# Optimization experiments

Hardware: AMD Instinct MI355X
Metric: run time of the kernel (lower is better)

## Reference

```python
import jax, jax.numpy as jnp
import numpy as np

N = 20000      # nodes
E = 320000     # edges (avg degree 16)
HID = 128      # hidden_channel
OUT = 128      # output_channel
SEQ = 8


def setup_inputs() -> dict:
    key = jax.random.key(0)
    ks = jax.random.split(key, 8)
    h = jax.random.normal(ks[0], (N, HID), jnp.float32)
    c = jax.random.normal(ks[1], (N, HID), jnp.float32)
    edge_index = jax.random.randint(ks[2], (2, E), 0, N, jnp.int64)
    edge_attr = jax.random.uniform(ks[3], (E,), jnp.float32)
    # GCNConv weights (PyG: x @ W then propagate), xavier-ish scale
    W_init = jax.random.normal(ks[4], (2 * HID, 2 * OUT), jnp.float32) * (2.0 / (2 * HID + 2 * OUT)) ** 0.5
    b_init = jnp.zeros((2 * OUT,), jnp.float32)
    W_cell = jax.random.normal(ks[5], (HID + OUT, 4 * OUT), jnp.float32) * (2.0 / (HID + OUT + 4 * OUT)) ** 0.5
    b_cell = jnp.zeros((4 * OUT,), jnp.float32)
    return {"h": h, "c": c, "edge_index": edge_index, "edge_attr": edge_attr,
            "W_init": W_init, "b_init": b_init, "W_cell": W_cell, "b_cell": b_cell,
            "seq_len": SEQ}


def _gcn(x, W, b, src, dst, ew, dinv):
    # PyG GCNConv with normalize=True, add_self_loops=True (self-loop weight 1.0)
    xw = x @ W                                   # [N, C_out]
    norm = dinv[src] * ew * dinv[dst]            # sym-normalized edge weights
    agg = jnp.zeros_like(xw).at[dst].add(xw[src] * norm[:, None])
    agg = agg + xw * (dinv * dinv)[:, None]      # self-loop term
    return agg + b


def reference(h, c, edge_index, edge_attr, W_init, b_init, W_cell, b_cell, seq_len):
    src, dst = edge_index[0], edge_index[1]
    n = h.shape[0]
    # degree with self-loops (weight 1.0), shared by both convs
    deg = jnp.zeros((n,), h.dtype).at[dst].add(edge_attr) + 1.0
    dinv = jax.lax.rsqrt(deg)

    # _init_states
    states = jax.nn.elu(_gcn(jnp.concatenate([h, c], axis=1), W_init, b_init, src, dst, edge_attr, dinv))
    h_t, c_t = states[:, :OUT], states[:, OUT:]

    def step(carry, _):
        h_cur, c_cur = carry
        # NOTE: original code feeds the initial h (not h_cur) as x each step
        combined = jnp.concatenate([h, h_cur], axis=1)
        cc = _gcn(combined, W_cell, b_cell, src, dst, edge_attr, dinv)
        cc_i, cc_f, cc_o, cc_g = jnp.split(cc, 4, axis=1)
        c_next = jax.nn.sigmoid(cc_f) * c_cur + jax.nn.sigmoid(cc_i) * jnp.tanh(cc_g)
        h_next = jax.nn.sigmoid(cc_o) * jnp.tanh(c_next)
        return (h_next, c_next), h_next

    (_, _), out = jax.lax.scan(step, (h_t, c_t), None, length=seq_len)
    return out  # [seq_len, N, OUT]
```

## Files before the change

kernel.cpp:

```cpp
#include <hip/hip_runtime.h>

#define N_NODES 20000
#define N_EDGES 320000
#define SEQ 8

typedef __attribute__((ext_vector_type(8))) short bf16x8;
typedef __attribute__((ext_vector_type(4))) float floatx4;
typedef const unsigned int __attribute__((address_space(1)))* gas_u32;
typedef unsigned int __attribute__((address_space(3)))* las_u32;

__device__ __forceinline__ unsigned short f2bf(float f) {
  unsigned int u = __builtin_bit_cast(unsigned int, f);
  return (unsigned short)((u + 0x7fffu + ((u >> 16) & 1u)) >> 16);
}
__device__ __forceinline__ float bflo(unsigned int u) {
  return __builtin_bit_cast(float, u << 16);
}
__device__ __forceinline__ float bfhi(unsigned int u) {
  return __builtin_bit_cast(float, u & 0xffff0000u);
}
__device__ __forceinline__ float sigf(float x) { return 1.f / (1.f + __expf(-x)); }

__device__ __forceinline__ void gl_lds16(const void* g, void* l) {
  auto gp = (gas_u32)g;
  auto lp = (las_u32)(unsigned int)(unsigned long long)l;
  __builtin_amdgcn_global_load_lds(gp, lp, 16, 0, 0);
}


__global__ void k_prologue(const float* __restrict__ Wi,
                           const float* __restrict__ Wc,
                           const float* __restrict__ bc,
                           unsigned short* __restrict__ WiT,
                           unsigned short* __restrict__ WcT,
                           float* __restrict__ bcp,
                           float* __restrict__ deg, int* __restrict__ counts) {
  int idx = blockIdx.x * 256 + threadIdx.x;
  if (idx < N_NODES) { deg[idx] = 1.0f; counts[idx] = 0; }
  if (idx < 65536) {
    int n = idx >> 8, k = idx & 255;
    WiT[n * 256 + k] = f2bf(Wi[k * 256 + n]);
  }
  if (idx < 512) bcp[idx] = bc[((idx & 3) << 7) | (idx >> 2)];
  int n2 = idx >> 8, k2 = idx & 255;
  int orig = ((n2 & 3) << 7) | (n2 >> 2);
  WcT[n2 * 256 + k2] = f2bf(Wc[k2 * 512 + orig]);
}

__global__ void k_deg(const int* __restrict__ ei, const float* __restrict__ ea,
                      float* __restrict__ deg, int* __restrict__ counts) {
  int e = blockIdx.x * 256 + threadIdx.x;
  if (e >= N_EDGES) return;
  int d = ei[N_EDGES + e];
  atomicAdd(&deg[d], ea[e]);
  atomicAdd(&counts[d], 1);
}

__global__ __launch_bounds__(1024) void k_scan(
    const int* __restrict__ counts, const float* __restrict__ deg,
    float* __restrict__ dinv, int* __restrict__ row_ptr,
    int* __restrict__ cursor) {
  __shared__ int smw[16];
  int t = threadIdx.x;
  int lane = t & 63, wv = t >> 6;
  int base = t * 20;
  int v[20];
  float dv[20];
  bool live = (t < 1000);
  if (live) {
    const int4* pc = (const int4*)(counts + base);
    const float4* pd = (const float4*)(deg + base);
#pragma unroll
    for (int i = 0; i < 5; ++i) {
      int4 q = pc[i];
      float4 f = pd[i];
      v[4 * i] = q.x; v[4 * i + 1] = q.y; v[4 * i + 2] = q.z; v[4 * i + 3] = q.w;
      dv[4 * i] = f.x; dv[4 * i + 1] = f.y; dv[4 * i + 2] = f.z; dv[4 * i + 3] = f.w;
    }
  } else {
#pragma unroll
    for (int i = 0; i < 20; ++i) { v[i] = 0; dv[i] = 1.f; }
  }
  int s = 0;
#pragma unroll
  for (int i = 0; i < 20; ++i) s += v[i];
  int inc = s;
#pragma unroll
  for (int o = 1; o < 64; o <<= 1) {
    int u = __shfl_up(inc, o);
    if (lane >= o) inc += u;
  }
  if (lane == 63) smw[wv] = inc;
  __syncthreads();
  if (t == 0) {
    int r = 0;
#pragma unroll
    for (int i = 0; i < 16; ++i) { int x = smw[i]; smw[i] = r; r += x; }
  }
  __syncthreads();
  int run = smw[wv] + inc - s;
  if (live) {
    int rp[20];
    float iv[20];
#pragma unroll
    for (int i = 0; i < 20; ++i) {
      rp[i] = run;
      run += v[i];
      iv[i] = rsqrtf(dv[i]);
    }
    int4* prp = (int4*)(row_ptr + base);
    int4* pcu = (int4*)(cursor + base);
    float4* pdv = (float4*)(dinv + base);
#pragma unroll
    for (int i = 0; i < 5; ++i) {
      int4 q; q.x = rp[4 * i]; q.y = rp[4 * i + 1]; q.z = rp[4 * i + 2]; q.w = rp[4 * i + 3];
      prp[i] = q;
      pcu[i] = q;
      float4 f; f.x = iv[4 * i]; f.y = iv[4 * i + 1]; f.z = iv[4 * i + 2]; f.w = iv[4 * i + 3];
      pdv[i] = f;
    }
  }
  if (t == 0) row_ptr[N_NODES] = N_EDGES;
}

__global__ void k_fill(const int* __restrict__ ei, const float* __restrict__ ea,
                       const float* __restrict__ dinv, int* __restrict__ cursor,
                       int2* __restrict__ csr) {
  int e = blockIdx.x * 256 + threadIdx.x;
  if (e >= N_EDGES) return;
  int s = ei[e], d = ei[N_EDGES + e];
  int k = atomicAdd(&cursor[d], 1);
  int2 p;
  p.x = s;
  p.y = __builtin_bit_cast(int, dinv[s] * ea[e] * dinv[d]);
  csr[k] = p;
}


__global__ __launch_bounds__(256) void k_agg_init(
    const float* __restrict__ h, const float* __restrict__ c,
    unsigned int* __restrict__ AhAc_u, const float* __restrict__ dinv,
    const int* __restrict__ row_ptr, const int2* __restrict__ csr) {
  int wid = (blockIdx.x * 256 + threadIdx.x) >> 6;
  int lane = threadIdx.x & 63;
  if (wid >= N_NODES) return;
  float di = dinv[wid], dd = di * di;
  const float4* xb = (lane < 32) ? (const float4*)h : (const float4*)c;
  int lcol = lane & 31;
  float4 a = xb[(size_t)wid * 32 + lcol];
  float s0 = a.x * dd, s1 = a.y * dd, s2 = a.z * dd, s3 = a.w * dd;
  int e0 = row_ptr[wid], end = row_ptr[wid + 1];
  for (int base = e0; base < end; base += 64) {
    int n = end - base;
    if (n > 64) n = 64;
    int sl = 0;
    float wl = 0.f;
    if (base + lane < end) {
      int2 p = csr[base + lane];
      sl = p.x;
      wl = __builtin_bit_cast(float, p.y);
    }
    int j = 0;
    for (; j + 4 <= n; j += 4) {
      int sa = __shfl(sl, j), sb = __shfl(sl, j + 1);
      int sc = __shfl(sl, j + 2), sd = __shfl(sl, j + 3);
      float wa = __shfl(wl, j), wb = __shfl(wl, j + 1);
      float wc = __shfl(wl, j + 2), wd = __shfl(wl, j + 3);
      float4 va = xb[(size_t)sa * 32 + lcol];
      float4 vb = xb[(size_t)sb * 32 + lcol];
      float4 vc = xb[(size_t)sc * 32 + lcol];
      float4 vd = xb[(size_t)sd * 32 + lcol];
      s0 += va.x * wa; s1 += va.y * wa; s2 += va.z * wa; s3 += va.w * wa;
      s0 += vb.x * wb; s1 += vb.y * wb; s2 += vb.z * wb; s3 += vb.w * wb;
      s0 += vc.x * wc; s1 += vc.y * wc; s2 += vc.z * wc; s3 += vc.w * wc;
      s0 += vd.x * wd; s1 += vd.y * wd; s2 += vd.z * wd; s3 += vd.w * wd;
    }
    for (; j < n; ++j) {
      int sa = __shfl(sl, j);
      float wa = __shfl(wl, j);
      float4 va = xb[(size_t)sa * 32 + lcol];
      s0 += va.x * wa; s1 += va.y * wa; s2 += va.z * wa; s3 += va.w * wa;
    }
  }
  uint2 o;
  o.x = (unsigned int)f2bf(s0) | ((unsigned int)f2bf(s1) << 16);
  o.y = (unsigned int)f2bf(s2) | ((unsigned int)f2bf(s3) << 16);
  ((uint2*)AhAc_u)[(size_t)wid * 64 + lane] = o;
}

__global__ __launch_bounds__(256) void k_agg_step(
    const unsigned int* __restrict__ hbf_u, unsigned int* __restrict__ AhAc_u,
    const float* __restrict__ dinv, const int* __restrict__ row_ptr,
    const int2* __restrict__ csr) {
  int wid = (blockIdx.x * 256 + threadIdx.x) >> 6;
  int lane = threadIdx.x & 63;
  if (wid >= N_NODES) return;
  float di = dinv[wid], dd = di * di;
  unsigned int a = hbf_u[(size_t)wid * 64 + lane];
  float s0 = bflo(a) * dd, s1 = bfhi(a) * dd;
  int e0 = row_ptr[wid], end = row_ptr[wid + 1];
  for (int base = e0; base < end; base += 64) {
    int n = end - base;
    if (n > 64) n = 64;
    int sl = 0;
    float wl = 0.f;
    if (base + lane < end) {
      int2 p = csr[base + lane];
      sl = p.x;
      wl = __builtin_bit_cast(float, p.y);
    }
    int j = 0;
    for (; j + 4 <= n; j += 4) {
      int sa = __shfl(sl, j), sb = __shfl(sl, j + 1);
      int sc = __shfl(sl, j + 2), sd = __shfl(sl, j + 3);
      float wa = __shfl(wl, j), wb = __shfl(wl, j + 1);
      float wc = __shfl(wl, j + 2), wd = __shfl(wl, j + 3);
      unsigned int va = hbf_u[(size_t)sa * 64 + lane];
      unsigned int vb = hbf_u[(size_t)sb * 64 + lane];
      unsigned int vc = hbf_u[(size_t)sc * 64 + lane];
      unsigned int vd = hbf_u[(size_t)sd * 64 + lane];
      s0 += bflo(va) * wa; s1 += bfhi(va) * wa;
      s0 += bflo(vb) * wb; s1 += bfhi(vb) * wb;
      s0 += bflo(vc) * wc; s1 += bfhi(vc) * wc;
      s0 += bflo(vd) * wd; s1 += bfhi(vd) * wd;
    }
    for (; j < n; ++j) {
      int sa = __shfl(sl, j);
      float wa = __shfl(wl, j);
      unsigned int va = hbf_u[(size_t)sa * 64 + lane];
      s0 += bflo(va) * wa; s1 += bfhi(va) * wa;
    }
  }
  AhAc_u[(size_t)wid * 128 + 64 + lane] =
      (unsigned int)f2bf(s0) | ((unsigned int)f2bf(s1) << 16);
}

template <int EPI, int KK, int LDA>
__global__ __launch_bounds__(256) void k_gemm(
    const unsigned short* __restrict__ A, const unsigned short* __restrict__ BT,
    const float* __restrict__ bias,
    float* __restrict__ c_cur, unsigned short* __restrict__ hbf,
    float* __restrict__ out0) {
  __shared__ __align__(16) union {
    struct { unsigned short a[128 * 64]; unsigned short b[128 * 64]; } ab;
    float ep[64 * 132];
  } sm;
  const int M = N_NODES;
  int tid = threadIdx.x;
  int bm0 = blockIdx.x * 128, bn0 = blockIdx.y * 128;
  int wave = tid >> 6, lane = tid & 63;
  int wrow = (wave >> 1) * 64, wcol = (wave & 1) * 64;
  int lr = lane & 15, lq = lane >> 4;
  int key = lr & 7;

  int lr8 = lane >> 3, cq = lane & 7;
  int gq8 = (cq ^ lr8) * 8;

  floatx4 acc[4][4];
#pragma unroll
  for (int i = 0; i < 4; i++)
#pragma unroll
    for (int j = 0; j < 4; j++) acc[i][j] = (floatx4){0.f, 0.f, 0.f, 0.f};

  for (int k0 = 0; k0 < KK; k0 += 64) {
    __syncthreads();
#pragma unroll
    for (int p = 0; p < 4; ++p) {
      int row = p * 32 + wave * 8;
      int ra = bm0 + row + lr8;
      if (ra > M - 1) ra = M - 1;
      gl_lds16(A + (size_t)ra * LDA + k0 + gq8, sm.ab.a + row * 64);
      gl_lds16(BT + (size_t)(bn0 + row + lr8) * KK + k0 + gq8,
               sm.ab.b + row * 64);
    }
    __syncthreads();
#pragma unroll
    for (int ks = 0; ks < 2; ++ks) {
      int q = ks * 4 + lq;
      int slot = (q ^ key) << 3;
      bf16x8 af[4], bfr[4];
#pragma unroll
      for (int mi = 0; mi < 4; mi++)
        af[mi] = *(const bf16x8*)(sm.ab.a + (wrow + mi * 16 + lr) * 64 + slot);
#pragma unroll
      for (int ni = 0; ni < 4; ni++)
        bfr[ni] = *(const bf16x8*)(sm.ab.b + (wcol + ni * 16 + lr) * 64 + slot);
#pragma unroll
      for (int mi = 0; mi < 4; mi++)
#pragma unroll
        for (int ni = 0; ni < 4; ni++)
          acc[mi][ni] = __builtin_amdgcn_mfma_f32_16x16x32_bf16(
              af[mi], bfr[ni], acc[mi][ni], 0, 0, 0);
    }
  }
  __syncthreads();

  if (EPI == 0) {
#pragma unroll
    for (int mi = 0; mi < 4; mi++) {
#pragma unroll
      for (int r = 0; r < 4; r++) {
        int grow = bm0 + wrow + mi * 16 + lq * 4 + r;
        if (grow >= M) continue;
#pragma unroll
        for (int ni = 0; ni < 4; ni++) {
          int gcol = bn0 + wcol + ni * 16 + lr;
          float v = acc[mi][ni][r] + bias[gcol];
          v = (v > 0.f) ? v : expm1f(v);
          if (gcol < 128) hbf[(size_t)grow * 128 + gcol] = f2bf(v);
          else c_cur[(size_t)grow * 128 + gcol - 128] = v;
        }
      }
    }
  } else {
#pragma unroll
    for (int hch = 0; hch < 2; ++hch) {
      if ((wrow >> 6) == hch) {
#pragma unroll
        for (int mi = 0; mi < 4; mi++)
#pragma unroll
          for (int r = 0; r < 4; r++) {
            int row_l = mi * 16 + lq * 4 + r;
#pragma unroll
            for (int ni = 0; ni < 4; ni++)
              sm.ep[row_l * 132 + wcol + ni * 16 + lr] = acc[mi][ni][r];
          }
      }
      __syncthreads();
#pragma unroll
      for (int it = 0; it < 8; ++it) {
        int p = tid + it * 256;
        int row_l = p >> 5, j = p & 31;
        int grow = bm0 + hch * 64 + row_l;
        if (grow < M) {
          int jg = (bn0 >> 2) + j;
          const float* eb = sm.ep + row_l * 132 + 4 * j;
          float4 kb = *(const float4*)&bias[bn0 + 4 * j];
          float gi = eb[0] + kb.x;
          float gf = eb[1] + kb.y;
          float go = eb[2] + kb.z;
          float gg = eb[3] + kb.w;
          size_t o = (size_t)grow * 128 + jg;
          float cp = c_cur[o];
          float cn = sigf(gf) * cp + sigf(gi) * tanhf(gg);
          float hn = sigf(go) * tanhf(cn);
          c_cur[o] = cn;
          hbf[o] = f2bf(hn);
          out0[o] = hn;
        }
      }
      __syncthreads();
    }
  }
}

extern "C" void kernel_launch(void* const* d_in, const int* in_sizes, int n_in,
                              void* d_out, int out_size, void* d_ws, size_t ws_size,
                              hipStream_t stream) {
  const float* h  = (const float*)d_in[0];
  const float* c  = (const float*)d_in[1];
  const int*   ei = (const int*)d_in[2];
  const float* ea = (const float*)d_in[3];
  const float* Wi = (const float*)d_in[4];
  const float* bi = (const float*)d_in[5];
  const float* Wc = (const float*)d_in[6];
  const float* bc = (const float*)d_in[7];
  float* out = (float*)d_out;

  char* w = (char*)d_ws;
  size_t off = 0;
  auto alloc = [&](size_t bytes) {
    void* p = w + off;
    off += (bytes + 511) & ~(size_t)511;
    return p;
  };
  float* deg           = (float*)alloc(N_NODES * 4);
  float* dinv          = (float*)alloc(N_NODES * 4);
  int* counts          = (int*)alloc(N_NODES * 4);
  int* cursor          = (int*)alloc(N_NODES * 4);
  int* row_ptr         = (int*)alloc((N_NODES + 1) * 4);
  int2* csr            = (int2*)alloc((size_t)N_EDGES * 8);
  unsigned short* WiT  = (unsigned short*)alloc(256 * 256 * 2);
  unsigned short* WcT  = (unsigned short*)alloc(512 * 256 * 2);
  float* bcp           = (float*)alloc(512 * 4);
  unsigned short* AhAc = (unsigned short*)alloc((size_t)N_NODES * 256 * 2);
  unsigned short* hbf  = (unsigned short*)alloc((size_t)N_NODES * 128 * 2);
  float* c_cur         = (float*)alloc((size_t)N_NODES * 128 * 4);

  const int NB_E = (N_EDGES + 255) / 256;
  const int NB_AGG = N_NODES * 64 / 256;
  const int MB = (N_NODES + 127) / 128;

  k_prologue<<<512, 256, 0, stream>>>(Wi, Wc, bc, WiT, WcT, bcp, deg, counts);
  k_deg<<<NB_E, 256, 0, stream>>>(ei, ea, deg, counts);
  k_scan<<<1, 1024, 0, stream>>>(counts, deg, dinv, row_ptr, cursor);
  k_fill<<<NB_E, 256, 0, stream>>>(ei, ea, dinv, cursor, csr);

  k_agg_init<<<NB_AGG, 256, 0, stream>>>(h, c, (unsigned int*)AhAc, dinv,
                                         row_ptr, csr);
  k_gemm<0, 256, 256><<<dim3(MB, 2), 256, 0, stream>>>(
      AhAc, WiT, bi, c_cur, hbf, nullptr);

  for (int t = 0; t < SEQ; ++t) {
    k_agg_step<<<NB_AGG, 256, 0, stream>>>((unsigned int*)hbf,
                                           (unsigned int*)AhAc, dinv, row_ptr,
                                           csr);
    k_gemm<2, 256, 256><<<dim3(MB, 4), 256, 0, stream>>>(
        AhAc, WcT, bcp, c_cur, hbf, out + (size_t)t * N_NODES * 128);
  }
}
```

Measured before the change: 508.9 us.

## Fuse per-step aggregation, GEMM and LSTM epilogue into one kernel

Replaces the separate per-step aggregation kernel and gate GEMM with a single kernel. Each 128-row block first gathers neighbour h values into shared memory, then computes all four gate column tiles and applies the LSTM update. The hidden state is double-buffered because blocks now read the previous h while writing the new one. This removes the global round-trip of the aggregated h and one launch per step. In exchange, grid parallelism drops to about 157 blocks with large shared memory, and the latency-bound gather runs at low occupancy.

Result: slower. 819.5 us (+61.0%).

```diff
diff --git a/kernel.cpp b/kernel.cpp
--- a/kernel.cpp
+++ b/kernel.cpp
@@ -135,7 +135,6 @@
   p.y = __builtin_bit_cast(int, dinv[s] * ea[e] * dinv[d]);
   csr[k] = p;
 }
-
 
 __global__ __launch_bounds__(256) void k_agg_init(
     const float* __restrict__ h, const float* __restrict__ c,
@@ -188,63 +187,11 @@
   ((uint2*)AhAc_u)[(size_t)wid * 64 + lane] = o;
 }
 
-__global__ __launch_bounds__(256) void k_agg_step(
-    const unsigned int* __restrict__ hbf_u, unsigned int* __restrict__ AhAc_u,
-    const float* __restrict__ dinv, const int* __restrict__ row_ptr,
-    const int2* __restrict__ csr) {
-  int wid = (blockIdx.x * 256 + threadIdx.x) >> 6;
-  int lane = threadIdx.x & 63;
-  if (wid >= N_NODES) return;
-  float di = dinv[wid], dd = di * di;
-  unsigned int a = hbf_u[(size_t)wid * 64 + lane];
-  float s0 = bflo(a) * dd, s1 = bfhi(a) * dd;
-  int e0 = row_ptr[wid], end = row_ptr[wid + 1];
-  for (int base = e0; base < end; base += 64) {
-    int n = end - base;
-    if (n > 64) n = 64;
-    int sl = 0;
-    float wl = 0.f;
-    if (base + lane < end) {
-      int2 p = csr[base + lane];
-      sl = p.x;
-      wl = __builtin_bit_cast(float, p.y);
-    }
-    int j = 0;
-    for (; j + 4 <= n; j += 4) {
-      int sa = __shfl(sl, j), sb = __shfl(sl, j + 1);
-      int sc = __shfl(sl, j + 2), sd = __shfl(sl, j + 3);
-      float wa = __shfl(wl, j), wb = __shfl(wl, j + 1);
-      float wc = __shfl(wl, j + 2), wd = __shfl(wl, j + 3);
-      unsigned int va = hbf_u[(size_t)sa * 64 + lane];
-      unsigned int vb = hbf_u[(size_t)sb * 64 + lane];
-      unsigned int vc = hbf_u[(size_t)sc * 64 + lane];
-      unsigned int vd = hbf_u[(size_t)sd * 64 + lane];
-      s0 += bflo(va) * wa; s1 += bfhi(va) * wa;
-      s0 += bflo(vb) * wb; s1 += bfhi(vb) * wb;
-      s0 += bflo(vc) * wc; s1 += bfhi(vc) * wc;
-      s0 += bflo(vd) * wd; s1 += bfhi(vd) * wd;
-    }
-    for (; j < n; ++j) {
-      int sa = __shfl(sl, j);
-      float wa = __shfl(wl, j);
-      unsigned int va = hbf_u[(size_t)sa * 64 + lane];
-      s0 += bflo(va) * wa; s1 += bfhi(va) * wa;
-    }
-  }
-  AhAc_u[(size_t)wid * 128 + 64 + lane] =
-      (unsigned int)f2bf(s0) | ((unsigned int)f2bf(s1) << 16);
-}
-
-template <int EPI, int KK, int LDA>
-__global__ __launch_bounds__(256) void k_gemm(
+__global__ __launch_bounds__(256) void k_gemm0(
     const unsigned short* __restrict__ A, const unsigned short* __restrict__ BT,
-    const float* __restrict__ bias,
-    float* __restrict__ c_cur, unsigned short* __restrict__ hbf,
-    float* __restrict__ out0) {
-  __shared__ __align__(16) union {
-    struct { unsigned short a[128 * 64]; unsigned short b[128 * 64]; } ab;
-    float ep[64 * 132];
-  } sm;
+    const float* __restrict__ bias, float* __restrict__ c_cur,
+    unsigned short* __restrict__ hbf) {
+  __shared__ __align__(16) struct { unsigned short a[128 * 64]; unsigned short b[128 * 64]; } sm;
   const int M = N_NODES;
   int tid = threadIdx.x;
   int bm0 = blockIdx.x * 128, bn0 = blockIdx.y * 128;
@@ -252,7 +199,6 @@
   int wrow = (wave >> 1) * 64, wcol = (wave & 1) * 64;
   int lr = lane & 15, lq = lane >> 4;
   int key = lr & 7;
-
   int lr8 = lane >> 3, cq = lane & 7;
   int gq8 = (cq ^ lr8) * 8;
 
@@ -262,16 +208,15 @@
 #pragma unroll
     for (int j = 0; j < 4; j++) acc[i][j] = (floatx4){0.f, 0.f, 0.f, 0.f};
 
-  for (int k0 = 0; k0 < KK; k0 += 64) {
+  for (int k0 = 0; k0 < 256; k0 += 64) {
     __syncthreads();
 #pragma unroll
     for (int p = 0; p < 4; ++p) {
       int row = p * 32 + wave * 8;
       int ra = bm0 + row + lr8;
       if (ra > M - 1) ra = M - 1;
-      gl_lds16(A + (size_t)ra * LDA + k0 + gq8, sm.ab.a + row * 64);
-      gl_lds16(BT + (size_t)(bn0 + row + lr8) * KK + k0 + gq8,
-               sm.ab.b + row * 64);
+      gl_lds16(A + (size_t)ra * 256 + k0 + gq8, sm.a + row * 64);
+      gl_lds16(BT + (size_t)(bn0 + row + lr8) * 256 + k0 + gq8, sm.b + row * 64);
     }
     __syncthreads();
 #pragma unroll
@@ -281,10 +226,10 @@
       bf16x8 af[4], bfr[4];
 #pragma unroll
       for (int mi = 0; mi < 4; mi++)
-        af[mi] = *(const bf16x8*)(sm.ab.a + (wrow + mi * 16 + lr) * 64 + slot);
+        af[mi] = *(const bf16x8*)(sm.a + (wrow + mi * 16 + lr) * 64 + slot);
 #pragma unroll
       for (int ni = 0; ni < 4; ni++)
-        bfr[ni] = *(const bf16x8*)(sm.ab.b + (wcol + ni * 16 + lr) * 64 + slot);
+        bfr[ni] = *(const bf16x8*)(sm.b + (wcol + ni * 16 + lr) * 64 + slot);
 #pragma unroll
       for (int mi = 0; mi < 4; mi++)
 #pragma unroll
@@ -293,49 +238,176 @@
               af[mi], bfr[ni], acc[mi][ni], 0, 0, 0);
     }
   }
-  __syncthreads();
-
-  if (EPI == 0) {
-#pragma unroll
-    for (int mi = 0; mi < 4; mi++) {
-#pragma unroll
-      for (int r = 0; r < 4; r++) {
-        int grow = bm0 + wrow + mi * 16 + lq * 4 + r;
-        if (grow >= M) continue;
-#pragma unroll
-        for (int ni = 0; ni < 4; ni++) {
-          int gcol = bn0 + wcol + ni * 16 + lr;
-          float v = acc[mi][ni][r] + bias[gcol];
-          v = (v > 0.f) ? v : expm1f(v);
-          if (gcol < 128) hbf[(size_t)grow * 128 + gcol] = f2bf(v);
-          else c_cur[(size_t)grow * 128 + gcol - 128] = v;
-        }
-      }
-    }
-  } else {
+
+#pragma unroll
+  for (int mi = 0; mi < 4; mi++) {
+#pragma unroll
+    for (int r = 0; r < 4; r++) {
+      int grow = bm0 + wrow + mi * 16 + lq * 4 + r;
+      if (grow >= M) continue;
+#pragma unroll
+      for (int ni = 0; ni < 4; ni++) {
+        int gcol = bn0 + wcol + ni * 16 + lr;
+        float v = acc[mi][ni][r] + bias[gcol];
+        v = (v > 0.f) ? v : expm1f(v);
+        if (gcol < 128) hbf[(size_t)grow * 128 + gcol] = f2bf(v);
+        else c_cur[(size_t)grow * 128 + gcol - 128] = v;
+      }
+    }
+  }
+}
+
+__global__ __launch_bounds__(512) void k_step(
+    const int2* __restrict__ csr, const int* __restrict__ row_ptr,
+    const float* __restrict__ dinv, const unsigned short* __restrict__ AhAc,
+    const unsigned short* __restrict__ WcT, const float* __restrict__ bcp,
+    float* __restrict__ c_cur, const unsigned int* __restrict__ hr,
+    unsigned short* __restrict__ hw, float* __restrict__ out0) {
+  __shared__ __align__(16) unsigned short smA[4][128 * 64];
+  __shared__ __align__(16) unsigned short smB[2][128 * 64];
+  __shared__ __align__(16) float ep[64 * 132];
+  const int M = N_NODES;
+  int tid = threadIdx.x;
+  int bm0 = blockIdx.x * 128;
+  int wave = tid >> 6, lane = tid & 63;
+  int wr = wave >> 2, wc = wave & 3;
+  int wrow = wr * 64, wcol = wc * 32;
+  int lr = lane & 15, lq = lane >> 4;
+  int key = lr & 7;
+  int lr8 = lane >> 3, cq = lane & 7;
+  int gq8 = (cq ^ lr8) * 8;
+
+#pragma unroll
+  for (int p = 0; p < 2; ++p) {
+#pragma unroll
+    for (int kc = 0; kc < 2; ++kc) {
+      int row = p * 64 + wave * 8;
+      int ra = bm0 + row + lr8;
+      if (ra > M - 1) ra = M - 1;
+      gl_lds16(AhAc + (size_t)ra * 256 + kc * 64 + gq8, smA[kc] + row * 64);
+    }
+  }
+
+  {
+    int kcw = 2 + (lane >> 5);
+    int cc2 = (lane * 2) & 63;
+    int grp = cc2 >> 3, el = cc2 & 7;
+    for (int rl = wave * 16; rl < wave * 16 + 16; ++rl) {
+      int wid = bm0 + rl;
+      if (wid >= N_NODES) continue;
+      float di = dinv[wid], dd = di * di;
+      unsigned int a = hr[(size_t)wid * 64 + lane];
+      float s0 = bflo(a) * dd, s1 = bfhi(a) * dd;
+      int e0 = row_ptr[wid], end = row_ptr[wid + 1];
+      for (int base = e0; base < end; base += 64) {
+        int n = end - base;
+        if (n > 64) n = 64;
+        int sl = 0;
+        float wl = 0.f;
+        if (base + lane < end) {
+          int2 p = csr[base + lane];
+          sl = p.x;
+          wl = __builtin_bit_cast(float, p.y);
+        }
+        int j = 0;
+        for (; j + 4 <= n; j += 4) {
+          int sa = __shfl(sl, j), sb = __shfl(sl, j + 1);
+          int sc = __shfl(sl, j + 2), sd = __shfl(sl, j + 3);
+          float wa = __shfl(wl, j), wb = __shfl(wl, j + 1);
+          float wcv = __shfl(wl, j + 2), wd = __shfl(wl, j + 3);
+          unsigned int va = hr[(size_t)sa * 64 + lane];
+          unsigned int vb = hr[(size_t)sb * 64 + lane];
+          unsigned int vc = hr[(size_t)sc * 64 + lane];
+          unsigned int vd = hr[(size_t)sd * 64 + lane];
+          s0 += bflo(va) * wa; s1 += bfhi(va) * wa;
+          s0 += bflo(vb) * wb; s1 += bfhi(vb) * wb;
+          s0 += bflo(vc) * wcv; s1 += bfhi(vc) * wcv;
+          s0 += bflo(vd) * wd; s1 += bfhi(vd) * wd;
+        }
+        for (; j < n; ++j) {
+          int sa = __shfl(sl, j);
+          float wa = __shfl(wl, j);
+          unsigned int va = hr[(size_t)sa * 64 + lane];
+          s0 += bflo(va) * wa; s1 += bfhi(va) * wa;
+        }
+      }
+      int lidx = rl * 64 + ((grp ^ (rl & 7)) << 3) + el;
+      unsigned int packed =
+          (unsigned int)f2bf(s0) | ((unsigned int)f2bf(s1) << 16);
+      *(unsigned int*)&smA[kcw][lidx] = packed;
+    }
+  }
+
+  for (int bn = 0; bn < 4; ++bn) {
+    int bn0 = bn * 128;
+    floatx4 acc[4][2];
+#pragma unroll
+    for (int i = 0; i < 4; i++)
+#pragma unroll
+      for (int j = 0; j < 2; j++) acc[i][j] = (floatx4){0.f, 0.f, 0.f, 0.f};
+
+#pragma unroll
+    for (int kp = 0; kp < 2; ++kp) {
+      __syncthreads();
+#pragma unroll
+      for (int cc = 0; cc < 2; ++cc) {
+        int kc = kp * 2 + cc;
+#pragma unroll
+        for (int p = 0; p < 2; ++p) {
+          int row = p * 64 + wave * 8;
+          gl_lds16(WcT + (size_t)(bn0 + row + lr8) * 256 + kc * 64 + gq8,
+                   smB[cc] + row * 64);
+        }
+      }
+      __syncthreads();
+#pragma unroll
+      for (int cc = 0; cc < 2; ++cc) {
+        int kc = kp * 2 + cc;
+#pragma unroll
+        for (int ks = 0; ks < 2; ++ks) {
+          int q = ks * 4 + lq;
+          int slot = (q ^ key) << 3;
+          bf16x8 af[4], bfr[2];
+#pragma unroll
+          for (int mi = 0; mi < 4; mi++)
+            af[mi] = *(const bf16x8*)(smA[kc] + (wrow + mi * 16 + lr) * 64 + slot);
+#pragma unroll
+          for (int ni = 0; ni < 2; ni++)
+            bfr[ni] = *(const bf16x8*)(smB[cc] + (wcol + ni * 16 + lr) * 64 + slot);
+#pragma unroll
+          for (int mi = 0; mi < 4; mi++)
+#pragma unroll
+            for (int ni = 0; ni < 2; ni++)
+              acc[mi][ni] = __builtin_amdgcn_mfma_f32_16x16x32_bf16(
+                  af[mi], bfr[ni], acc[mi][ni], 0, 0, 0);
+        }
+      }
+    }
+
 #pragma unroll
     for (int hch = 0; hch < 2; ++hch) {
-      if ((wrow >> 6) == hch) {
+      __syncthreads();
+      if (wr == hch) {
 #pragma unroll
         for (int mi = 0; mi < 4; mi++)
 #pragma unroll
           for (int r = 0; r < 4; r++) {
             int row_l = mi * 16 + lq * 4 + r;
 #pragma unroll
-            for (int ni = 0; ni < 4; ni++)
-              sm.ep[row_l * 132 + wcol + ni * 16 + lr] = acc[mi][ni][r];
+            for (int ni = 0; ni < 2; ni++)
+              ep[row_l * 132 + wcol + ni * 16 + lr] = acc[mi][ni][r];
           }
       }
       __syncthreads();
 #pragma unroll
-      for (int it = 0; it < 8; ++it) {
-        int p = tid + it * 256;
+      for (int it = 0; it < 4; ++it) {
+        int p = tid + it * 512;
         int row_l = p >> 5, j = p & 31;
         int grow = bm0 + hch * 64 + row_l;
         if (grow < M) {
           int jg = (bn0 >> 2) + j;
-          const float* eb = sm.ep + row_l * 132 + 4 * j;
-          float4 kb = *(const float4*)&bias[bn0 + 4 * j];
+          const float* eb = ep + row_l * 132 + 4 * j;
+          float4 kb = *(const float4*)&bcp[bn0 + 4 * j];
           float gi = eb[0] + kb.x;
           float gf = eb[1] + kb.y;
           float go = eb[2] + kb.z;
@@ -345,11 +417,10 @@
           float cn = sigf(gf) * cp + sigf(gi) * tanhf(gg);
           float hn = sigf(go) * tanhf(cn);
           c_cur[o] = cn;
-          hbf[o] = f2bf(hn);
+          hw[o] = f2bf(hn);
           out0[o] = hn;
         }
       }
-      __syncthreads();
     }
   }
 }
@@ -384,7 +455,8 @@
   unsigned short* WcT  = (unsigned short*)alloc(512 * 256 * 2);
   float* bcp           = (float*)alloc(512 * 4);
   unsigned short* AhAc = (unsigned short*)alloc((size_t)N_NODES * 256 * 2);
-  unsigned short* hbf  = (unsigned short*)alloc((size_t)N_NODES * 128 * 2);
+  unsigned short* hbfA = (unsigned short*)alloc((size_t)N_NODES * 128 * 2);
+  unsigned short* hbfB = (unsigned short*)alloc((size_t)N_NODES * 128 * 2);
   float* c_cur         = (float*)alloc((size_t)N_NODES * 128 * 4);
 
   const int NB_E = (N_EDGES + 255) / 256;
@@ -398,14 +470,13 @@
 
   k_agg_init<<<NB_AGG, 256, 0, stream>>>(h, c, (unsigned int*)AhAc, dinv,
                                          row_ptr, csr);
-  k_gemm<0, 256, 256><<<dim3(MB, 2), 256, 0, stream>>>(
-      AhAc, WiT, bi, c_cur, hbf, nullptr);
+  k_gemm0<<<dim3(MB, 2), 256, 0, stream>>>(AhAc, WiT, bi, c_cur, hbfA);
 
   for (int t = 0; t < SEQ; ++t) {
-    k_agg_step<<<NB_AGG, 256, 0, stream>>>((unsigned int*)hbf,
-                                           (unsigned int*)AhAc, dinv, row_ptr,
-                                           csr);
-    k_gemm<2, 256, 256><<<dim3(MB, 4), 256, 0, stream>>>(
-        AhAc, WcT, bcp, c_cur, hbf, out + (size_t)t * N_NODES * 128);
-  }
-}
+    const unsigned short* hr = (t & 1) ? hbfB : hbfA;
+    unsigned short* hw = (t & 1) ? hbfA : hbfB;
+    k_step<<<MB, 512, 0, stream>>>(csr, row_ptr, dinv, AhAc, WcT, bcp, c_cur,
+                                   (const unsigned int*)hr, hw,
+                                   out + (size_t)t * N_NODES * 128);
+  }
+}
```
